# Performance work log

Measured on AMD Instinct MI355X. Metric: run time of the kernel, lower is better.

The kernel has to match this reference:

```python
import jax, jax.numpy as jnp
import numpy as np

B, D, NUM_HOP, NUM_REL = 8192, 512, 8, 2000  # batch, input_dim, num_hop, num_relation
TAU = 1.0


def setup_inputs() -> dict:
    key = jax.random.key(0)
    ks = jax.random.split(key, 7)
    s = 1.0 / np.sqrt(D)  # PyTorch GRU uniform init bound
    return {
        "query": jax.random.normal(ks[0], (B, D), jnp.float32),
        "W_ih": jax.random.uniform(ks[1], (3 * D, D), jnp.float32, -s, s),
        "W_hh": jax.random.uniform(ks[2], (3 * D, D), jnp.float32, -s, s),
        "b_ih": jax.random.uniform(ks[3], (3 * D,), jnp.float32, -s, s),
        "b_hh": jax.random.uniform(ks[4], (3 * D,), jnp.float32, -s, s),
        "relation": jax.random.normal(ks[5], (2 * NUM_REL, D), jnp.float32),
        "eos": jax.random.normal(ks[6], (1, D), jnp.float32),
    }


def gru_cell(x, h, W_ih, W_hh, b_ih, b_hh):
    # PyTorch nn.GRU cell, gate order (r, z, n)
    gi = x @ W_ih.T + b_ih  # [B, 3D]
    gh = h @ W_hh.T + b_hh  # [B, 3D]
    ir, iz, i_n = jnp.split(gi, 3, axis=-1)
    hr, hz, h_n = jnp.split(gh, 3, axis=-1)
    r = jax.nn.sigmoid(ir + hr)
    z = jax.nn.sigmoid(iz + hz)
    n = jnp.tanh(i_n + r * h_n)
    return (1.0 - z) * n + z * h


def reference(query, W_ih, W_hh, b_ih, b_hh, relation, eos):
    # gru over seq [query, eos] starting from h0 = 0; hidden[1:] == final hx for 1 layer
    h0 = jnp.zeros_like(query)
    h1 = gru_cell(query, h0, W_ih, W_hh, b_ih, b_hh)
    hidden = gru_cell(jnp.broadcast_to(eos, query.shape), h1, W_ih, W_hh, b_ih, b_hh)

    def step(h, _):
        score = jnp.einsum('bd,rd->br', h, relation)          # [B, 2R]
        attention = jax.nn.softmax(score / TAU, axis=-1)
        subgoal = jnp.einsum('br,rd->bd', attention, relation)  # [B, D]
        h_new = gru_cell(subgoal, h, W_ih, W_hh, b_ih, b_hh)
        return h_new, subgoal

    _, subgoals = jax.lax.scan(step, hidden, None, length=NUM_HOP)  # [NUM_HOP, B, D]
    subgoals = jnp.moveaxis(subgoals, 0, 1)  # [B, NUM_HOP, D]
    masks = jnp.ones(subgoals.shape[:-1], dtype=bool)
    return subgoals, masks
```

## Files before the change

kernel.cpp:

```cpp
#include <hip/hip_runtime.h>


typedef _Float16 f16;
typedef _Float16 f16x8 __attribute__((ext_vector_type(8)));
typedef _Float16 f16x4 __attribute__((ext_vector_type(4)));
typedef float    f32x4 __attribute__((ext_vector_type(4)));

constexpr int BATCH = 8192;
constexpr int DDIM  = 512;
constexpr int D3    = 1536;
constexpr int NRELT = 4000;
constexpr int NRELP = 4096;
constexpr int NHOP  = 8;

#define MFMA16(a,b,c) __builtin_amdgcn_mfma_f32_16x16x32_f16((a),(b),(c),0,0,0)

__device__ __forceinline__ void gll16(const void* g, void* l) {
  __builtin_amdgcn_global_load_lds(
      (const __attribute__((address_space(1))) unsigned int*)g,
      (__attribute__((address_space(3))) unsigned int*)l, 16, 0, 0);
}

__global__ __launch_bounds__(256) void k_split(const float* __restrict__ src,
                                               f16* __restrict__ hi, f16* __restrict__ lo, int n) {
  int i = blockIdx.x * 256 + threadIdx.x;
  if (i >= n) return;
  float v = src[i];
  f16 h = (f16)v;
  hi[i] = h;
  lo[i] = (f16)(v - (float)h);
}

__global__ __launch_bounds__(256) void k_prep_rel(const float* __restrict__ rel,
    f16* __restrict__ rhi, f16* __restrict__ rlo,
    f16* __restrict__ thi, f16* __restrict__ tlo) {
  int i = blockIdx.x * 256 + threadIdx.x;
  if (i >= NRELP * DDIM) return;
  int r = i >> 9, d = i & 511;
  float v = (r < NRELT) ? rel[i] : 0.f;
  f16 h = (f16)v, l = (f16)(v - (float)h);
  rhi[i] = h; rlo[i] = l;
  thi[(size_t)d * NRELP + r] = h;
  tlo[(size_t)d * NRELP + r] = l;
}

__global__ __launch_bounds__(64) void k_gieos(const float* __restrict__ W,
                                              const float* __restrict__ eos,
                                              float* __restrict__ out) {
  int o = blockIdx.x;
  float s = 0.f;
  for (int i = threadIdx.x; i < DDIM; i += 64) s += W[(size_t)o * DDIM + i] * eos[i];
  for (int off = 32; off; off >>= 1) s += __shfl_xor(s, off);
  if (threadIdx.x == 0) out[o] = s;
}

template<int EPI>
__global__ __launch_bounds__(256, 2)
void gemm_k(const f16* __restrict__ Ahi, const f16* __restrict__ Alo, int lda,
            const f16* __restrict__ Bhi, const f16* __restrict__ Blo, int ldb,
            float* __restrict__ Cout, f16* __restrict__ Chi, f16* __restrict__ Clo,
            int ldc, int K)
{
  __shared__ f16 lAh[128][32];
  __shared__ f16 lAl[128][32];
  __shared__ f16 lBh[128][32];
  __shared__ f16 lBl[128][32];

  const int tid  = threadIdx.x;
  const int lane = tid & 63;
  const int wave = tid >> 6;
  const int wm = wave >> 1;
  const int wn = wave & 1;
  const int m0 = blockIdx.x * 128;
  const int n0 = blockIdx.y * 128;
  const int rb = lane & 15;
  const int ko = (lane >> 4) * 8;

  const int kst = blockIdx.z * K;
  Cout += (size_t)blockIdx.z * (size_t)gridDim.x * 128 * (size_t)ldc;

  f32x4 acc[4][4] = {};

  for (int k0 = kst; k0 < kst + K; k0 += 32) {
    #pragma unroll
    for (int c = 0; c < 2; ++c) {
      const int ch = wave + c * 4;
      const int r  = ch * 16 + (lane >> 2);
      const size_t goff = (size_t)(n0 + r) * ldb + k0 + (lane & 3) * 8;
      gll16(Bhi + goff, &lBh[ch * 16][0]);
      gll16(Blo + goff, &lBl[ch * 16][0]);
    }
    #pragma unroll
    for (int c = 0; c < 2; ++c) {
      const int ch = wave + c * 4;
      const int r  = ch * 16 + (lane >> 2);
      const size_t goff = (size_t)(m0 + r) * lda + k0 + (lane & 3) * 8;
      gll16(Ahi + goff, &lAh[ch * 16][0]);
      gll16(Alo + goff, &lAl[ch * 16][0]);
    }
    __syncthreads();

    f16x8 ah[4], al[4], bh[4], bl[4];
    #pragma unroll
    for (int f = 0; f < 4; ++f) {
      ah[f] = *(const f16x8*)&lAh[wm * 64 + f * 16 + rb][ko];
      al[f] = *(const f16x8*)&lAl[wm * 64 + f * 16 + rb][ko];
      bh[f] = *(const f16x8*)&lBh[wn * 64 + f * 16 + rb][ko];
      bl[f] = *(const f16x8*)&lBl[wn * 64 + f * 16 + rb][ko];
    }
    #pragma unroll
    for (int fm = 0; fm < 4; ++fm)
      #pragma unroll
      for (int fn = 0; fn < 4; ++fn) {
        acc[fm][fn] = MFMA16(ah[fm], bh[fn], acc[fm][fn]);
        acc[fm][fn] = MFMA16(ah[fm], bl[fn], acc[fm][fn]);
        acc[fm][fn] = MFMA16(al[fm], bh[fn], acc[fm][fn]);
      }
    __syncthreads();
  }

  #pragma unroll
  for (int fm = 0; fm < 4; ++fm)
    #pragma unroll
    for (int fn = 0; fn < 4; ++fn)
      #pragma unroll
      for (int r = 0; r < 4; ++r) {
        const int gr = m0 + wm * 64 + fm * 16 + (lane >> 4) * 4 + r;
        const int gc = n0 + wn * 64 + fn * 16 + rb;
        const float v = acc[fm][fn][r];
        if constexpr (EPI == 0) {
          Cout[(size_t)gr * ldc + gc] = v;
        } else {
          const f16 vh = (f16)v;
          Chi[(size_t)gr * ldc + gc] = vh;
          Clo[(size_t)gr * ldc + gc] = (f16)(v - (float)vh);
        }
      }
}

__global__ __launch_bounds__(256)
void k_softmax(f16* __restrict__ Shi, f16* __restrict__ Slo) {
  const int row = blockIdx.x;
  f16* phi = Shi + (size_t)row * NRELP;
  f16* plo = Slo + (size_t)row * NRELP;
  const int tid = threadIdx.x, lane = tid & 63, wv = tid >> 6;
  const int ng = (tid < 232) ? 4 : 3;
  f32x4 v[4];
  float mx = -3.402823e38f;
  #pragma unroll
  for (int i = 0; i < 4; ++i)
    if (i < ng) {
      f16x4 hv = *(const f16x4*)(phi + (tid + 256 * i) * 4);
      f16x4 lv = *(const f16x4*)(plo + (tid + 256 * i) * 4);
      #pragma unroll
      for (int j = 0; j < 4; ++j) v[i][j] = (float)hv[j] + (float)lv[j];
      mx = fmaxf(fmaxf(fmaxf(mx, v[i][0]), fmaxf(v[i][1], v[i][2])), v[i][3]);
    }
  float l = 0.f;
  #pragma unroll
  for (int i = 0; i < 4; ++i)
    if (i < ng)
      l += __expf(v[i][0] - mx) + __expf(v[i][1] - mx)
         + __expf(v[i][2] - mx) + __expf(v[i][3] - mx);
  #pragma unroll
  for (int off = 1; off < 64; off <<= 1) {
    float om = __shfl_xor(mx, off), ol = __shfl_xor(l, off);
    float nm = fmaxf(mx, om);
    l = l * __expf(mx - nm) + ol * __expf(om - nm);
    mx = nm;
  }
  __shared__ float sm[4], sl[4];
  if (lane == 0) { sm[wv] = mx; sl[wv] = l; }
  __syncthreads();
  const float fm = fmaxf(fmaxf(sm[0], sm[1]), fmaxf(sm[2], sm[3]));
  const float fl = sl[0] * __expf(sm[0] - fm) + sl[1] * __expf(sm[1] - fm)
                 + sl[2] * __expf(sm[2] - fm) + sl[3] * __expf(sm[3] - fm);
  const float il = 1.f / fl;
  #pragma unroll
  for (int i = 0; i < 4; ++i)
    if (i < ng) {
      f16x4 oh, ol;
      #pragma unroll
      for (int j = 0; j < 4; ++j) {
        const float pv = __expf(v[i][j] - fm) * il;
        const f16 ph = (f16)pv;
        oh[j] = ph;
        ol[j] = (f16)(pv - (float)ph);
      }
      *(f16x4*)(phi + (tid + 256 * i) * 4) = oh;
      *(f16x4*)(plo + (tid + 256 * i) * 4) = ol;
    }
  if (tid < 24) {
    f16x4 z = {(f16)0.f, (f16)0.f, (f16)0.f, (f16)0.f};
    *(f16x4*)(phi + (1000 + tid) * 4) = z;
    *(f16x4*)(plo + (1000 + tid) * 4) = z;
  }
}

__global__ __launch_bounds__(256)
void k_subred(const float* __restrict__ Cp, float* __restrict__ outp,
              f16* __restrict__ xhi, f16* __restrict__ xlo, int hop) {
  const int idx = blockIdx.x * 256 + threadIdx.x;
  const int b = idx >> 7, d4 = (idx & 127) * 4;
  const size_t o = (size_t)b * DDIM + d4;
  f32x4 s = *(const f32x4*)(Cp + o);
  s += *(const f32x4*)(Cp + (size_t)BATCH * DDIM + o);
  s += *(const f32x4*)(Cp + 2 * (size_t)BATCH * DDIM + o);
  s += *(const f32x4*)(Cp + 3 * (size_t)BATCH * DDIM + o);
  *(f32x4*)(outp + (size_t)b * (NHOP * DDIM) + (size_t)hop * DDIM + d4) = s;
  f16x4 vh, vl;
  #pragma unroll
  for (int j = 0; j < 4; ++j) {
    const f16 ph = (f16)s[j];
    vh[j] = ph;
    vl[j] = (f16)(s[j] - (float)ph);
  }
  *(f16x4*)(xhi + o) = vh;
  *(f16x4*)(xlo + o) = vl;
}

__global__ __launch_bounds__(256)
void k_gates(const float* __restrict__ gi, const float* __restrict__ givec,
             const float* __restrict__ gh,
             const float* __restrict__ bih, const float* __restrict__ bhh,
             const float* __restrict__ hin, float* __restrict__ hout,
             f16* __restrict__ hhi, f16* __restrict__ hlo)
{
  const int idx = blockIdx.x * 256 + threadIdx.x;
  const int b  = idx >> 7;
  const int d4 = (idx & 127) * 4;
  f32x4 ir, iz, inn;
  if (gi) {
    const float* g = gi + (size_t)b * D3 + d4;
    ir  = *(const f32x4*)(g);
    iz  = *(const f32x4*)(g + DDIM);
    inn = *(const f32x4*)(g + 2 * DDIM);
  } else {
    ir  = *(const f32x4*)(givec + d4);
    iz  = *(const f32x4*)(givec + DDIM + d4);
    inn = *(const f32x4*)(givec + 2 * DDIM + d4);
  }
  ir  += *(const f32x4*)(bih + d4);
  iz  += *(const f32x4*)(bih + DDIM + d4);
  inn += *(const f32x4*)(bih + 2 * DDIM + d4);
  f32x4 hr = {0.f, 0.f, 0.f, 0.f}, hz = {0.f, 0.f, 0.f, 0.f}, hn = {0.f, 0.f, 0.f, 0.f};
  if (gh) {
    const float* g = gh + (size_t)b * D3 + d4;
    hr = *(const f32x4*)(g);
    hz = *(const f32x4*)(g + DDIM);
    hn = *(const f32x4*)(g + 2 * DDIM);
  }
  hr += *(const f32x4*)(bhh + d4);
  hz += *(const f32x4*)(bhh + DDIM + d4);
  hn += *(const f32x4*)(bhh + 2 * DDIM + d4);
  f32x4 hp = {0.f, 0.f, 0.f, 0.f};
  if (hin) hp = *(const f32x4*)(hin + (size_t)b * DDIM + d4);
  f32x4 hv; f16x4 vh, vl;
  #pragma unroll
  for (int j = 0; j < 4; ++j) {
    const float r = 1.f / (1.f + __expf(-(ir[j] + hr[j])));
    const float z = 1.f / (1.f + __expf(-(iz[j] + hz[j])));
    const float n = tanhf(inn[j] + r * hn[j]);
    const float h = (1.f - z) * n + z * hp[j];
    hv[j] = h;
    const f16 ph = (f16)h;
    vh[j] = ph;
    vl[j] = (f16)(h - (float)ph);
  }
  *(f32x4*)(hout + (size_t)b * DDIM + d4) = hv;
  *(f16x4*)(hhi + (size_t)b * DDIM + d4) = vh;
  *(f16x4*)(hlo + (size_t)b * DDIM + d4) = vl;
}

__global__ __launch_bounds__(256) void k_ones(float* __restrict__ o, int n) {
  int i = blockIdx.x * 256 + threadIdx.x;
  if (i < n) o[i] = 1.0f;
}

extern "C" void kernel_launch(void* const* d_in, const int* in_sizes, int n_in,
                              void* d_out, int out_size, void* d_ws, size_t ws_size,
                              hipStream_t stream)
{
  const float* query = (const float*)d_in[0];
  const float* W_ih  = (const float*)d_in[1];
  const float* W_hh  = (const float*)d_in[2];
  const float* b_ih  = (const float*)d_in[3];
  const float* b_hh  = (const float*)d_in[4];
  const float* rel   = (const float*)d_in[5];
  const float* eos   = (const float*)d_in[6];
  float* out = (float*)d_out;
  (void)in_sizes; (void)n_in; (void)out_size; (void)ws_size;

  char* w = (char*)d_ws;
  f16* SPhi    = (f16*)w;   w += (size_t)BATCH * NRELP * 2;
  f16* SPlo    = (f16*)w;   w += (size_t)BATCH * NRELP * 2;
  float* Cpart = (float*)w; w += (size_t)4 * BATCH * DDIM * 4;
  float* hbuf  = (float*)w; w += (size_t)BATCH * DDIM * 4;
  f16* h_hi    = (f16*)w;   w += (size_t)BATCH * DDIM * 2;
  f16* h_lo    = (f16*)w;   w += (size_t)BATCH * DDIM * 2;
  f16* x_hi    = (f16*)w;   w += (size_t)BATCH * DDIM * 2;
  f16* x_lo    = (f16*)w;   w += (size_t)BATCH * DDIM * 2;
  f16* wih_hi  = (f16*)w;   w += (size_t)D3 * DDIM * 2;
  f16* wih_lo  = (f16*)w;   w += (size_t)D3 * DDIM * 2;
  f16* whh_hi  = (f16*)w;   w += (size_t)D3 * DDIM * 2;
  f16* whh_lo  = (f16*)w;   w += (size_t)D3 * DDIM * 2;
  f16* rel_hi  = (f16*)w;   w += (size_t)NRELP * DDIM * 2;
  f16* rel_lo  = (f16*)w;   w += (size_t)NRELP * DDIM * 2;
  f16* relT_hi = (f16*)w;   w += (size_t)DDIM * NRELP * 2;
  f16* relT_lo = (f16*)w;   w += (size_t)DDIM * NRELP * 2;
  float* gieos = (float*)w; w += (size_t)D3 * 4;
  float* gi = (float*)SPhi;
  float* gh = (float*)SPhi + (size_t)BATCH * D3;

  k_split<<<(BATCH * DDIM + 255) / 256, 256, 0, stream>>>(query, x_hi, x_lo, BATCH * DDIM);
  k_split<<<(D3 * DDIM + 255) / 256, 256, 0, stream>>>(W_ih, wih_hi, wih_lo, D3 * DDIM);
  k_split<<<(D3 * DDIM + 255) / 256, 256, 0, stream>>>(W_hh, whh_hi, whh_lo, D3 * DDIM);
  k_prep_rel<<<(NRELP * DDIM + 255) / 256, 256, 0, stream>>>(rel, rel_hi, rel_lo, relT_hi, relT_lo);
  k_gieos<<<D3, 64, 0, stream>>>(W_ih, eos, gieos);

  const int ggrid = BATCH * DDIM / 4 / 256;

  gemm_k<0><<<dim3(64, 12), 256, 0, stream>>>(x_hi, x_lo, DDIM, wih_hi, wih_lo, DDIM,
      gi, nullptr, nullptr, D3, DDIM);
  k_gates<<<ggrid, 256, 0, stream>>>(gi, nullptr, nullptr, b_ih, b_hh, nullptr, hbuf, h_hi, h_lo);

  gemm_k<0><<<dim3(64, 12), 256, 0, stream>>>(h_hi, h_lo, DDIM, whh_hi, whh_lo, DDIM,
      gh, nullptr, nullptr, D3, DDIM);
  k_gates<<<ggrid, 256, 0, stream>>>(nullptr, gieos, gh, b_ih, b_hh, hbuf, hbuf, h_hi, h_lo);

  for (int hop = 0; hop < NHOP; ++hop) {
    gemm_k<1><<<dim3(64, 32), 256, 0, stream>>>(h_hi, h_lo, DDIM, rel_hi, rel_lo, DDIM,
        nullptr, SPhi, SPlo, NRELP, DDIM);
    k_softmax<<<BATCH, 256, 0, stream>>>(SPhi, SPlo);
    gemm_k<0><<<dim3(64, 4, 4), 256, 0, stream>>>(SPhi, SPlo, NRELP,
        relT_hi, relT_lo, NRELP, Cpart, nullptr, nullptr, DDIM, NRELP / 4);
    k_subred<<<ggrid, 256, 0, stream>>>(Cpart, out, x_hi, x_lo, hop);
    gemm_k<0><<<dim3(64, 12), 256, 0, stream>>>(x_hi, x_lo, DDIM, wih_hi, wih_lo, DDIM,
        gi, nullptr, nullptr, D3, DDIM);
    gemm_k<0><<<dim3(64, 12), 256, 0, stream>>>(h_hi, h_lo, DDIM, whh_hi, whh_lo, DDIM,
        gh, nullptr, nullptr, D3, DDIM);
    k_gates<<<ggrid, 256, 0, stream>>>(gi, nullptr, gh, b_ih, b_hh, hbuf, hbuf, h_hi, h_lo);
  }

  k_ones<<<(BATCH * NHOP + 255) / 256, 256, 0, stream>>>(out + (size_t)BATCH * NHOP * DDIM, BATCH * NHOP);
}
```

Baseline: 3.300 ms.

## Rewrite split-f16 GEMM as 256x256 double-buffered 8-wave kernel with swizzled LDS

Replaces the 128x128, 4-wave GEMM with a 256x256-tile, 8-wave kernel. It double-buffers LDS, prefetches the next K slice in four interleaved phases between MFMA groups, XOR-swizzles LDS rows to avoid bank conflicts, and raises wave priority around the MFMA blocks. Block IDs are remapped for XCD locality, and the two GRU gate GEMMs are merged into one launch. The goals are to hide global-load latency, reduce LDS conflicts and per-block overhead, and raise arithmetic intensity. In exchange it uses more LDS (128KB per block), more registers, fewer blocks per GEMM and more barriers per K-step.

```diff
diff --git a/kernel.cpp b/kernel.cpp
--- a/kernel.cpp
+++ b/kernel.cpp
@@ -14,6 +14,9 @@
 constexpr int NHOP  = 8;
 
 #define MFMA16(a,b,c) __builtin_amdgcn_mfma_f32_16x16x32_f16((a),(b),(c),0,0,0)
+#define BAR()   __builtin_amdgcn_s_barrier()
+#define FENCE() asm volatile("" ::: "memory")
+#define SCHED0() __builtin_amdgcn_sched_barrier(0)
 
 __device__ __forceinline__ void gll16(const void* g, void* l) {
   __builtin_amdgcn_global_load_lds(
@@ -55,77 +58,135 @@
 }
 
 template<int EPI>
-__global__ __launch_bounds__(256, 2)
-void gemm_k(const f16* __restrict__ Ahi, const f16* __restrict__ Alo, int lda,
-            const f16* __restrict__ Bhi, const f16* __restrict__ Blo, int ldb,
-            float* __restrict__ Cout, f16* __restrict__ Chi, f16* __restrict__ Clo,
-            int ldc, int K)
+__device__ __forceinline__ void gemm_core(
+    const f16* __restrict__ Ahi, const f16* __restrict__ Alo, int lda,
+    const f16* __restrict__ Bhi, const f16* __restrict__ Blo, int ldb,
+    float* __restrict__ Cout, f16* __restrict__ Chi, f16* __restrict__ Clo,
+    int ldc, int m0, int n0, int kst, int nt, f16* lds)
 {
-  __shared__ f16 lAh[128][32];
-  __shared__ f16 lAl[128][32];
-  __shared__ f16 lBh[128][32];
-  __shared__ f16 lBl[128][32];
-
   const int tid  = threadIdx.x;
   const int lane = tid & 63;
   const int wave = tid >> 6;
-  const int wm = wave >> 1;
-  const int wn = wave & 1;
-  const int m0 = blockIdx.x * 128;
-  const int n0 = blockIdx.y * 128;
+  const int wm = wave >> 2;
+  const int wn = wave & 3;
   const int rb = lane & 15;
-  const int ko = (lane >> 4) * 8;
-
-  const int kst = blockIdx.z * K;
-  Cout += (size_t)blockIdx.z * (size_t)gridDim.x * 128 * (size_t)ldc;
-
-  f32x4 acc[4][4] = {};
-
-  for (int k0 = kst; k0 < kst + K; k0 += 32) {
+  const int sl = lane >> 4;
+  const int srow = lane >> 2;
+
+  auto stage2 = [&](int buf, int p, int k0) {
+    const f16* src = (p == 0) ? Ahi : (p == 1) ? Alo : (p == 2) ? Bhi : Blo;
+    const int ld   = (p < 2) ? lda : ldb;
+    const int base = (p < 2) ? m0 : n0;
+    f16* pl = lds + ((buf * 4 + p) << 13);
     #pragma unroll
     for (int c = 0; c < 2; ++c) {
-      const int ch = wave + c * 4;
-      const int r  = ch * 16 + (lane >> 2);
-      const size_t goff = (size_t)(n0 + r) * ldb + k0 + (lane & 3) * 8;
-      gll16(Bhi + goff, &lBh[ch * 16][0]);
-      gll16(Blo + goff, &lBl[ch * 16][0]);
-    }
-    #pragma unroll
-    for (int c = 0; c < 2; ++c) {
-      const int ch = wave + c * 4;
-      const int r  = ch * 16 + (lane >> 2);
-      const size_t goff = (size_t)(m0 + r) * lda + k0 + (lane & 3) * 8;
-      gll16(Ahi + goff, &lAh[ch * 16][0]);
-      gll16(Alo + goff, &lAl[ch * 16][0]);
-    }
-    __syncthreads();
-
-    f16x8 ah[4], al[4], bh[4], bl[4];
+      const int r0 = wave * 16 + c * 128;
+      const int lr = r0 + srow;
+      const int slot = (lane & 3) ^ ((lr >> 1) & 3);
+      gll16(src + (size_t)(base + lr) * ld + k0 + slot * 8, pl + r0 * 32);
+    }
+  };
+  auto rd = [&](int buf, int p, int lr) -> f16x8 {
+    const int off = lr * 64 + ((sl ^ ((lr >> 1) & 3)) << 4);
+    return *(const f16x8*)((const char*)(lds + ((buf * 4 + p) << 13)) + off);
+  };
+
+  stage2(0, 0, kst); stage2(0, 1, kst); stage2(0, 2, kst); stage2(0, 3, kst);
+
+  f32x4 acc[8][4] = {};
+  f16x8 ah[4], al[4], bh0[2], bl0[2], bh1[2], bl1[2];
+
+  for (int t = 0; t < nt; ++t) {
+    const int cur = t & 1;
+    const bool more = (t + 1 < nt);
+    const int kn = kst + (t + 1) * 32;
+
+    asm volatile("s_waitcnt vmcnt(0)" ::: "memory");
+    BAR(); FENCE();
+    if (more) stage2(cur ^ 1, 0, kn);
     #pragma unroll
     for (int f = 0; f < 4; ++f) {
-      ah[f] = *(const f16x8*)&lAh[wm * 64 + f * 16 + rb][ko];
-      al[f] = *(const f16x8*)&lAl[wm * 64 + f * 16 + rb][ko];
-      bh[f] = *(const f16x8*)&lBh[wn * 64 + f * 16 + rb][ko];
-      bl[f] = *(const f16x8*)&lBl[wn * 64 + f * 16 + rb][ko];
-    }
-    #pragma unroll
-    for (int fm = 0; fm < 4; ++fm)
-      #pragma unroll
-      for (int fn = 0; fn < 4; ++fn) {
-        acc[fm][fn] = MFMA16(ah[fm], bh[fn], acc[fm][fn]);
-        acc[fm][fn] = MFMA16(ah[fm], bl[fn], acc[fm][fn]);
-        acc[fm][fn] = MFMA16(al[fm], bh[fn], acc[fm][fn]);
-      }
-    __syncthreads();
-  }
-
-  #pragma unroll
-  for (int fm = 0; fm < 4; ++fm)
+      ah[f] = rd(cur, 0, wm * 128 + f * 16 + rb);
+      al[f] = rd(cur, 1, wm * 128 + f * 16 + rb);
+    }
+    #pragma unroll
+    for (int n = 0; n < 2; ++n) {
+      bh0[n] = rd(cur, 2, wn * 64 + n * 16 + rb);
+      bl0[n] = rd(cur, 3, wn * 64 + n * 16 + rb);
+    }
+    FENCE(); BAR(); FENCE();
+    __builtin_amdgcn_s_setprio(1);
+    #pragma unroll
+    for (int f = 0; f < 4; ++f)
+      #pragma unroll
+      for (int n = 0; n < 2; ++n) {
+        acc[f][n] = MFMA16(ah[f], bh0[n], acc[f][n]);
+        acc[f][n] = MFMA16(ah[f], bl0[n], acc[f][n]);
+        acc[f][n] = MFMA16(al[f], bh0[n], acc[f][n]);
+      }
+    __builtin_amdgcn_s_setprio(0);
+    SCHED0();
+
+    if (more) stage2(cur ^ 1, 1, kn);
+    #pragma unroll
+    for (int n = 0; n < 2; ++n) {
+      bh1[n] = rd(cur, 2, wn * 64 + 32 + n * 16 + rb);
+      bl1[n] = rd(cur, 3, wn * 64 + 32 + n * 16 + rb);
+    }
+    FENCE(); BAR(); FENCE();
+    __builtin_amdgcn_s_setprio(1);
+    #pragma unroll
+    for (int f = 0; f < 4; ++f)
+      #pragma unroll
+      for (int n = 0; n < 2; ++n) {
+        acc[f][2 + n] = MFMA16(ah[f], bh1[n], acc[f][2 + n]);
+        acc[f][2 + n] = MFMA16(ah[f], bl1[n], acc[f][2 + n]);
+        acc[f][2 + n] = MFMA16(al[f], bh1[n], acc[f][2 + n]);
+      }
+    __builtin_amdgcn_s_setprio(0);
+    SCHED0();
+
+    if (more) stage2(cur ^ 1, 2, kn);
+    #pragma unroll
+    for (int f = 0; f < 4; ++f) {
+      ah[f] = rd(cur, 0, wm * 128 + 64 + f * 16 + rb);
+      al[f] = rd(cur, 1, wm * 128 + 64 + f * 16 + rb);
+    }
+    FENCE(); BAR(); FENCE();
+    __builtin_amdgcn_s_setprio(1);
+    #pragma unroll
+    for (int f = 0; f < 4; ++f)
+      #pragma unroll
+      for (int n = 0; n < 2; ++n) {
+        acc[4 + f][2 + n] = MFMA16(ah[f], bh1[n], acc[4 + f][2 + n]);
+        acc[4 + f][2 + n] = MFMA16(ah[f], bl1[n], acc[4 + f][2 + n]);
+        acc[4 + f][2 + n] = MFMA16(al[f], bh1[n], acc[4 + f][2 + n]);
+      }
+    __builtin_amdgcn_s_setprio(0);
+    SCHED0();
+
+    if (more) stage2(cur ^ 1, 3, kn);
+    FENCE(); BAR(); FENCE();
+    __builtin_amdgcn_s_setprio(1);
+    #pragma unroll
+    for (int f = 0; f < 4; ++f)
+      #pragma unroll
+      for (int n = 0; n < 2; ++n) {
+        acc[4 + f][n] = MFMA16(ah[f], bh0[n], acc[4 + f][n]);
+        acc[4 + f][n] = MFMA16(ah[f], bl0[n], acc[4 + f][n]);
+        acc[4 + f][n] = MFMA16(al[f], bh0[n], acc[4 + f][n]);
+      }
+    __builtin_amdgcn_s_setprio(0);
+    SCHED0();
+  }
+
+  #pragma unroll
+  for (int fm = 0; fm < 8; ++fm)
     #pragma unroll
     for (int fn = 0; fn < 4; ++fn)
       #pragma unroll
       for (int r = 0; r < 4; ++r) {
-        const int gr = m0 + wm * 64 + fm * 16 + (lane >> 4) * 4 + r;
+        const int gr = m0 + wm * 128 + fm * 16 + sl * 4 + r;
         const int gc = n0 + wn * 64 + fn * 16 + rb;
         const float v = acc[fm][fn][r];
         if constexpr (EPI == 0) {
@@ -138,6 +199,44 @@
       }
 }
 
+template<int EPI>
+__global__ __launch_bounds__(512, 2)
+void k_gemm8(const f16* __restrict__ Ahi, const f16* __restrict__ Alo, int lda,
+             const f16* __restrict__ Bhi, const f16* __restrict__ Blo, int ldb,
+             float* __restrict__ Cout, f16* __restrict__ Chi, f16* __restrict__ Clo,
+             int ldc, int K, int gy, int nblocks)
+{
+  __shared__ __align__(16) f16 lds[2 * 4 * 256 * 32];
+  const int bid = blockIdx.x;
+  const int id2 = (bid & 7) * (nblocks >> 3) + (bid >> 3);
+  const int m = id2 & 31;
+  const int rest = id2 >> 5;
+  const int n = rest % gy;
+  const int z = rest / gy;
+  float* Co = Cout ? Cout + (size_t)z * BATCH * (size_t)ldc : nullptr;
+  gemm_core<EPI>(Ahi, Alo, lda, Bhi, Blo, ldb, Co, Chi, Clo, ldc,
+                 m * 256, n * 256, z * K, K / 32, lds);
+}
+
+__global__ __launch_bounds__(512, 2)
+void k_gemm8_gru(const f16* __restrict__ xhi, const f16* __restrict__ xlo,
+                 const f16* __restrict__ hhi, const f16* __restrict__ hlo,
+                 const f16* __restrict__ wihhi, const f16* __restrict__ wihlo,
+                 const f16* __restrict__ whhhi, const f16* __restrict__ whhlo,
+                 float* __restrict__ gi, float* __restrict__ gh)
+{
+  __shared__ __align__(16) f16 lds[2 * 4 * 256 * 32];
+  const int bid = blockIdx.x;
+  const int id2 = (bid & 7) * 48 + (bid >> 3);
+  const int m = id2 & 31;
+  const int nn = id2 >> 5;
+  const bool second = nn >= 6;
+  gemm_core<0>(second ? hhi : xhi, second ? hlo : xlo, DDIM,
+               second ? whhhi : wihhi, second ? whhlo : wihlo, DDIM,
+               second ? gh : gi, nullptr, nullptr, D3,
+               m * 256, (second ? nn - 6 : nn) * 256, 0, DDIM / 32, lds);
+}
+
 __global__ __launch_bounds__(256)
 void k_softmax(f16* __restrict__ Shi, f16* __restrict__ Slo) {
   const int row = blockIdx.x;
@@ -169,12 +268,12 @@
     l = l * __expf(mx - nm) + ol * __expf(om - nm);
     mx = nm;
   }
-  __shared__ float sm[4], sl[4];
-  if (lane == 0) { sm[wv] = mx; sl[wv] = l; }
+  __shared__ float sm[4], slr[4];
+  if (lane == 0) { sm[wv] = mx; slr[wv] = l; }
   __syncthreads();
   const float fm = fmaxf(fmaxf(sm[0], sm[1]), fmaxf(sm[2], sm[3]));
-  const float fl = sl[0] * __expf(sm[0] - fm) + sl[1] * __expf(sm[1] - fm)
-                 + sl[2] * __expf(sm[2] - fm) + sl[3] * __expf(sm[3] - fm);
+  const float fl = slr[0] * __expf(sm[0] - fm) + slr[1] * __expf(sm[1] - fm)
+                 + slr[2] * __expf(sm[2] - fm) + slr[3] * __expf(sm[3] - fm);
   const float il = 1.f / fl;
   #pragma unroll
   for (int i = 0; i < 4; ++i)
@@ -320,25 +419,23 @@
 
   const int ggrid = BATCH * DDIM / 4 / 256;
 
-  gemm_k<0><<<dim3(64, 12), 256, 0, stream>>>(x_hi, x_lo, DDIM, wih_hi, wih_lo, DDIM,
-      gi, nullptr, nullptr, D3, DDIM);
+  k_gemm8<0><<<192, 512, 0, stream>>>(x_hi, x_lo, DDIM, wih_hi, wih_lo, DDIM,
+      gi, nullptr, nullptr, D3, DDIM, 6, 192);
   k_gates<<<ggrid, 256, 0, stream>>>(gi, nullptr, nullptr, b_ih, b_hh, nullptr, hbuf, h_hi, h_lo);
 
-  gemm_k<0><<<dim3(64, 12), 256, 0, stream>>>(h_hi, h_lo, DDIM, whh_hi, whh_lo, DDIM,
-      gh, nullptr, nullptr, D3, DDIM);
+  k_gemm8<0><<<192, 512, 0, stream>>>(h_hi, h_lo, DDIM, whh_hi, whh_lo, DDIM,
+      gh, nullptr, nullptr, D3, DDIM, 6, 192);
   k_gates<<<ggrid, 256, 0, stream>>>(nullptr, gieos, gh, b_ih, b_hh, hbuf, hbuf, h_hi, h_lo);
 
   for (int hop = 0; hop < NHOP; ++hop) {
-    gemm_k<1><<<dim3(64, 32), 256, 0, stream>>>(h_hi, h_lo, DDIM, rel_hi, rel_lo, DDIM,
-        nullptr, SPhi, SPlo, NRELP, DDIM);
+    k_gemm8<1><<<512, 512, 0, stream>>>(h_hi, h_lo, DDIM, rel_hi, rel_lo, DDIM,
+        nullptr, SPhi, SPlo, NRELP, DDIM, 16, 512);
     k_softmax<<<BATCH, 256, 0, stream>>>(SPhi, SPlo);
-    gemm_k<0><<<dim3(64, 4, 4), 256, 0, stream>>>(SPhi, SPlo, NRELP,
-        relT_hi, relT_lo, NRELP, Cpart, nullptr, nullptr, DDIM, NRELP / 4);
+    k_gemm8<0><<<256, 512, 0, stream>>>(SPhi, SPlo, NRELP,
+        relT_hi, relT_lo, NRELP, Cpart, nullptr, nullptr, DDIM, 1024, 2, 256);
     k_subred<<<ggrid, 256, 0, stream>>>(Cpart, out, x_hi, x_lo, hop);
-    gemm_k<0><<<dim3(64, 12), 256, 0, stream>>>(x_hi, x_lo, DDIM, wih_hi, wih_lo, DDIM,
-        gi, nullptr, nullptr, D3, DDIM);
-    gemm_k<0><<<dim3(64, 12), 256, 0, stream>>>(h_hi, h_lo, DDIM, whh_hi, whh_lo, DDIM,
-        gh, nullptr, nullptr, D3, DDIM);
+    k_gemm8_gru<<<384, 512, 0, stream>>>(x_hi, x_lo, h_hi, h_lo,
+        wih_hi, wih_lo, whh_hi, whh_lo, gi, gh);
     k_gates<<<ggrid, 256, 0, stream>>>(gi, nullptr, gh, b_ih, b_hh, hbuf, hbuf, h_hi, h_lo);
   }
 
```

Measured after the change: 3.331 ms. About the same (+0.9%).
